# Performance work log

Hardware: AMD Instinct MI355X
Metric: run time of the kernel (lower is better)

Reference implementation:

```python
import jax, jax.numpy as jnp
import numpy as np


def _min_gru_layer(h_in, Wz, bz, Wh, bh):
    # h_in: [B, T, D_in]; gates/candidate via two GEMMs
    z = jax.nn.sigmoid(jnp.einsum('btd,dh->bth', h_in, Wz) + bz)  # [B,T,H]
    h_tilde = jnp.einsum('btd,dh->bth', h_in, Wh) + bh            # [B,T,H]
    # Recurrence h_t = a_t * h_{t-1} + b_t with a_t = 1-z_t, b_t = z_t*h_tilde.
    # h_0 = 0 (frozen zeros param in the torch module), so the associative
    # scan over (a, b) directly yields h_t for t = 1..T.
    a = 1.0 - z
    b = z * h_tilde

    def combine(c1, c2):
        a1, b1 = c1
        a2, b2 = c2
        return a1 * a2, a2 * b1 + b2

    _, h = jax.lax.associative_scan(combine, (a, b), axis=1)
    return h


def setup_inputs() -> dict:
    key = jax.random.key(0)
    ks = jax.random.split(key, 8)
    B, T, Din, H, Dout = 8, 4096, 512, 1024, 512
    s_in = 1.0 / np.sqrt(Din)
    s_h = 1.0 / np.sqrt(H)
    return {
        'x':   jax.random.normal(ks[0], (B, T, Din), dtype=jnp.float32),
        'Wz0': jax.random.normal(ks[1], (Din, H), dtype=jnp.float32) * s_in,
        'bz0': jnp.zeros((H,), dtype=jnp.float32),
        'Wh0': jax.random.normal(ks[2], (Din, H), dtype=jnp.float32) * s_in,
        'bh0': jnp.zeros((H,), dtype=jnp.float32),
        'Wz1': jax.random.normal(ks[3], (H, H), dtype=jnp.float32) * s_h,
        'bz1': jnp.zeros((H,), dtype=jnp.float32),
        'Wh1': jax.random.normal(ks[4], (H, H), dtype=jnp.float32) * s_h,
        'bh1': jnp.zeros((H,), dtype=jnp.float32),
        'Wfc': jax.random.normal(ks[5], (H, Dout), dtype=jnp.float32) * s_h,
        'bfc': jnp.zeros((Dout,), dtype=jnp.float32),
    }


def reference(x, Wz0, bz0, Wh0, bh0, Wz1, bz1, Wh1, bh1, Wfc, bfc):
    h = _min_gru_layer(x, Wz0, bz0, Wh0, bh0)   # layer 0
    h = _min_gru_layer(h, Wz1, bz1, Wh1, bh1)   # layer 1
    return jnp.einsum('bth,ho->bto', h, Wfc) + bfc
```

## Files before the change

kernel.cpp:

```cpp
#include <hip/hip_runtime.h>

typedef __attribute__((ext_vector_type(4))) float fv4;
typedef __attribute__((ext_vector_type(8))) _Float16 hv8;
typedef __attribute__((ext_vector_type(4))) _Float16 hv4;
typedef __attribute__((ext_vector_type(2))) _Float16 hv2;

__device__ __forceinline__ void gload16(const void* g, void* l) {
  __builtin_amdgcn_global_load_lds(
      (const __attribute__((address_space(1))) unsigned int*)g,
      (__attribute__((address_space(3))) unsigned int*)l, 16, 0, 0);
}

struct GemmCore {
  const _Float16 *ap0, *bp0;
  size_t half;
  _Float16 *ldsA0, *ldsA1, *ldsB0, *ldsB1;
  const _Float16 *fa0, *fa1, *fb0, *fb1;
  int wave;

  __device__ __forceinline__ void init(const _Float16* A, const _Float16* Bt,
                                       _Float16* lds, int m0, int n0, int K,
                                       int tid) {
    wave = tid >> 6;
    const int lane = tid & 63;
    const int wm = (wave >> 1), wn = (wave & 1);
    const int quad = lane >> 4, r = lane & 15;
    ldsA0 = lds;         ldsA1 = lds + 4096;
    ldsB0 = lds + 8192;  ldsB1 = lds + 12288;
    const int cg = (tid & 3) ^ ((tid >> 3) & 3);
    ap0 = A  + (size_t)(m0 + (tid >> 2)) * K + cg * 8;
    bp0 = Bt + (size_t)(n0 + (tid >> 2)) * K + cg * 8;
    half = (size_t)64 * K;
    const int sq = quad ^ ((r >> 1) & 3);
    fa0 = ldsA0 + (wm * 64 + r) * 32 + sq * 8;
    fa1 = ldsA1 + (wm * 64 + r) * 32 + sq * 8;
    fb0 = ldsB0 + (wn * 64 + r) * 32 + sq * 8;
    fb1 = ldsB1 + (wn * 64 + r) * 32 + sq * 8;
  }

  __device__ __forceinline__ void run(fv4 acc[4][4], int K) {
    const int kiters = K >> 6;
    for (int kk = 0; kk < kiters; ++kk) {
      gload16(ap0,             ldsA0 + wave * 512);
      gload16(ap0 + half,      ldsA0 + wave * 512 + 2048);
      gload16(ap0 + 32,        ldsA1 + wave * 512);
      gload16(ap0 + half + 32, ldsA1 + wave * 512 + 2048);
      gload16(bp0,             ldsB0 + wave * 512);
      gload16(bp0 + half,      ldsB0 + wave * 512 + 2048);
      gload16(bp0 + 32,        ldsB1 + wave * 512);
      gload16(bp0 + half + 32, ldsB1 + wave * 512 + 2048);
      ap0 += 64; bp0 += 64;
      __syncthreads();

      hv8 av[4], bv[4];
#pragma unroll
      for (int t = 0; t < 4; ++t) {
        av[t] = *(const hv8*)(fa0 + t * 512);
        bv[t] = *(const hv8*)(fb0 + t * 512);
      }
#pragma unroll
      for (int tm = 0; tm < 4; ++tm)
#pragma unroll
        for (int tn = 0; tn < 4; ++tn)
          acc[tm][tn] = __builtin_amdgcn_mfma_f32_16x16x32_f16(av[tm], bv[tn],
                                                               acc[tm][tn], 0, 0, 0);
#pragma unroll
      for (int t = 0; t < 4; ++t) {
        av[t] = *(const hv8*)(fa1 + t * 512);
        bv[t] = *(const hv8*)(fb1 + t * 512);
      }
#pragma unroll
      for (int tm = 0; tm < 4; ++tm)
#pragma unroll
        for (int tn = 0; tn < 4; ++tn)
          acc[tm][tn] = __builtin_amdgcn_mfma_f32_16x16x32_f16(av[tm], bv[tn],
                                                               acc[tm][tn], 0, 0, 0);
      __syncthreads();
    }
  }
};

__device__ __forceinline__ void xcd_map(int bid, int ntl2, int mt_per_x,
                                        int& m0, int& n0) {
  const int xcd = bid & 7;
  const int k2  = bid >> 3;
  m0 = (xcd * mt_per_x + (k2 >> ntl2)) * 128;
  n0 = (k2 & ((1 << ntl2) - 1)) * 128;
}

__global__ __launch_bounds__(256)
void gemm_gate(const _Float16* __restrict__ A, const _Float16* __restrict__ Btf,
               _Float16* __restrict__ zh2,
               float* __restrict__ cA, float* __restrict__ cB,
               const float* __restrict__ bz, const float* __restrict__ bh,
               int K, int ntl2, int mt_per_x) {
  __shared__ _Float16 lds[4 * 128 * 32];
  const int tid  = threadIdx.x;
  const int lane = tid & 63;
  const int wave = tid >> 6;
  const int wm = wave >> 1, wn = wave & 1;
  const int quad = lane >> 4, r = lane & 15;
  int m0, n0;
  xcd_map(blockIdx.x, ntl2, mt_per_x, m0, n0);

  GemmCore core;
  core.init(A, Btf, lds, m0, n0, K, tid);
  fv4 acc[4][4] = {};
  core.run(acc, K);

  const int jb   = (n0 + wn * 64) >> 1;
  const int row0 = m0 + wm * 64 + quad * 4;
  const int cidx = (m0 >> 6) + wm;
#pragma unroll
  for (int tn = 0; tn < 2; ++tn) {
    const int j = jb + tn * 16 + r;
    const float bzv = bz[j];
    const float bhv = bh[j];
    float qA[4], qB[4];
#pragma unroll
    for (int tm = 0; tm < 4; ++tm) {
      float sA = 1.0f, sB = 0.0f;
#pragma unroll
      for (int r2 = 0; r2 < 4; ++r2) {
        const float zpre = acc[tm][tn][r2] + bzv;
        const float hpre = acc[tm][tn + 2][r2] + bhv;
        const float z = 1.0f / (1.0f + __expf(-zpre));
        const _Float16 a16 = (_Float16)(1.0f - z);
        const _Float16 b16 = (_Float16)(z * hpre);
        hv2 ab = {a16, b16};
        *(hv2*)(zh2 + ((size_t)(row0 + tm * 16 + r2) * 1024 + j) * 2) = ab;
        const float af = (float)a16, bf = (float)b16;
        sB = af * sB + bf;
        sA = sA * af;
      }
      qA[tm] = sA; qB[tm] = sB;
    }
#pragma unroll
    for (int tm = 0; tm < 4; ++tm) {
      float Av = qA[tm], Bv = qB[tm];
      float Ap = __shfl_up(Av, 16, 64);
      float Bp = __shfl_up(Bv, 16, 64);
      if (quad >= 1) { Bv = Av * Bp + Bv; Av = Ap * Av; }
      Ap = __shfl_up(Av, 32, 64);
      Bp = __shfl_up(Bv, 32, 64);
      if (quad >= 2) { Bv = Av * Bp + Bv; Av = Ap * Av; }
      qA[tm] = Av; qB[tm] = Bv;
    }
    if (quad == 3) {
      float CA = 1.0f, CB = 0.0f;
#pragma unroll
      for (int tm = 0; tm < 4; ++tm) { CB = qA[tm] * CB + qB[tm]; CA *= qA[tm]; }
      cA[(size_t)cidx * 1024 + j] = CA;
      cB[(size_t)cidx * 1024 + j] = CB;
    }
  }
}

__global__ __launch_bounds__(256)
void gemm_f16_bt(const _Float16* __restrict__ A, const _Float16* __restrict__ Bt,
                 float* __restrict__ C, const float* __restrict__ bias,
                 int N, int K, int ntl2, int mt_per_x) {
  __shared__ _Float16 lds[4 * 128 * 32];
  const int tid  = threadIdx.x;
  const int lane = tid & 63;
  const int wave = tid >> 6;
  const int wm = wave >> 1, wn = wave & 1;
  const int quad = lane >> 4, r = lane & 15;
  int m0, n0;
  xcd_map(blockIdx.x, ntl2, mt_per_x, m0, n0);

  GemmCore core;
  core.init(A, Bt, lds, m0, n0, K, tid);
  fv4 acc[4][4] = {};
  core.run(acc, K);

  const int col0 = n0 + wn * 64 + r;
  const int row0 = m0 + wm * 64 + quad * 4;
#pragma unroll
  for (int tn = 0; tn < 4; ++tn) {
    const int col = col0 + tn * 16;
    const float bs = bias[col];
#pragma unroll
    for (int tm = 0; tm < 4; ++tm) {
#pragma unroll
      for (int r2 = 0; r2 < 4; ++r2) {
        C[(size_t)(row0 + tm * 16 + r2) * N + col] = acc[tm][tn][r2] + bs;
      }
    }
  }
}

__global__ void cvt_f16(const float* __restrict__ x, _Float16* __restrict__ y) {
  size_t i = ((size_t)blockIdx.x * 256 + threadIdx.x) * 4;
  fv4 v = *(const fv4*)(x + i);
  *(hv4*)(y + i) = __builtin_convertvector(v, hv4);
}

__global__ void transpose_cvt(const float* __restrict__ W, _Float16* __restrict__ Wt,
                              int K, int N, int mult, int off) {
  __shared__ float tile[32][33];
  const int tx = threadIdx.x, ty = threadIdx.y;
  const int n  = blockIdx.x * 32 + tx;
  const int kb = blockIdx.y * 32;
  for (int i = ty; i < 32; i += 8)
    tile[i][tx] = W[(size_t)(kb + i) * N + n];
  __syncthreads();
  const int k = kb + tx;
  for (int i = ty; i < 32; i += 8)
    Wt[(size_t)(blockIdx.x * mult + off + i) * K + k] = (_Float16)tile[tx][i];
}

__global__ void scan_phaseB(const float* __restrict__ cA, const float* __restrict__ cB,
                            float* __restrict__ hcy) {
  const int gtid = blockIdx.x * 256 + threadIdx.x;
  const int lane = gtid & 63;
  const int wid  = gtid >> 6;
  const int h  = (wid & 255) * 4;
  const int bb = wid >> 8;
  const size_t o = (size_t)(bb * 64 + lane) * 1024 + h;
  fv4 Aa = *(const fv4*)(cA + o);
  fv4 Bv = *(const fv4*)(cB + o);
#pragma unroll
  for (int d = 1; d < 64; d <<= 1) {
    fv4 Ap, Bp;
#pragma unroll
    for (int k = 0; k < 4; ++k) {
      Ap[k] = __shfl_up(Aa[k], d, 64);
      Bp[k] = __shfl_up(Bv[k], d, 64);
    }
    if (lane >= d) {
      Bv = Aa * Bp + Bv;
      Aa = Ap * Aa;
    }
  }
  fv4 hc;
#pragma unroll
  for (int k = 0; k < 4; ++k) hc[k] = __shfl_up(Bv[k], 1, 64);
  if (lane == 0) { hc.x = 0.f; hc.y = 0.f; hc.z = 0.f; hc.w = 0.f; }
  *(fv4*)(hcy + o) = hc;
}

__global__ void scan_phaseC(const _Float16* __restrict__ zh2,
                            const float* __restrict__ hcy,
                            _Float16* __restrict__ hout) {
  const int idx = blockIdx.x * 256 + threadIdx.x;
  const int h  = (idx & 255) * 4;
  const int c  = (idx >> 8) & 63;
  const int bb = idx >> 14;
  const size_t base = ((size_t)(bb * 4096 + c * 64) * 1024 + h) * 2;
  const size_t ob   = (size_t)(bb * 4096 + c * 64) * 1024 + h;
  const size_t o    = (size_t)(bb * 64 + c) * 1024 + h;
  fv4 hc = *(const fv4*)(hcy + o);
#pragma unroll 4
  for (int t = 0; t < 64; ++t) {
    hv8 v = *(const hv8*)(zh2 + base + (size_t)t * 2048);
    fv4 av = __builtin_convertvector(__builtin_shufflevector(v, v, 0, 2, 4, 6), fv4);
    fv4 bv = __builtin_convertvector(__builtin_shufflevector(v, v, 1, 3, 5, 7), fv4);
    hc = av * hc + bv;
    *(hv4*)(hout + ob + (size_t)t * 1024) = __builtin_convertvector(hc, hv4);
  }
}

extern "C" void kernel_launch(void* const* d_in, const int* in_sizes, int n_in,
                              void* d_out, int out_size, void* d_ws, size_t ws_size,
                              hipStream_t stream) {
  const float* x   = (const float*)d_in[0];
  const float* Wz0 = (const float*)d_in[1];
  const float* bz0 = (const float*)d_in[2];
  const float* Wh0 = (const float*)d_in[3];
  const float* bh0 = (const float*)d_in[4];
  const float* Wz1 = (const float*)d_in[5];
  const float* bz1 = (const float*)d_in[6];
  const float* Wh1 = (const float*)d_in[7];
  const float* bh1 = (const float*)d_in[8];
  const float* Wfc = (const float*)d_in[9];
  const float* bfc = (const float*)d_in[10];

  const int Mrows = 32768;
  const int H = 1024, Din = 512, Dout = 512;

  char* w = (char*)d_ws;
  _Float16* zh2   = (_Float16*)w; w += (size_t)Mrows * 2 * H * 2;
  _Float16* hx    = (_Float16*)w; w += (size_t)Mrows * H * 2;
  _Float16* Wzh0t = (_Float16*)w; w += (size_t)2 * H * Din * 2;
  _Float16* Wzh1t = (_Float16*)w; w += (size_t)2 * H * H * 2;
  _Float16* Wft   = (_Float16*)w; w += (size_t)Dout * H * 2;
  float*    cA    = (float*)w;    w += (size_t)8 * 64 * H * 4;
  float*    cB    = (float*)w;    w += (size_t)8 * 64 * H * 4;
  float*    hcy   = (float*)w;    w += (size_t)8 * 64 * H * 4;
  _Float16* Xb    = hx;

  cvt_f16<<<Mrows * Din / 1024, 256, 0, stream>>>(x, Xb);
  transpose_cvt<<<dim3(H / 32, Din / 32), dim3(32, 8), 0, stream>>>(Wz0, Wzh0t, Din, H, 64, 0);
  transpose_cvt<<<dim3(H / 32, Din / 32), dim3(32, 8), 0, stream>>>(Wh0, Wzh0t, Din, H, 64, 32);
  transpose_cvt<<<dim3(H / 32, H / 32),   dim3(32, 8), 0, stream>>>(Wz1, Wzh1t, H, H, 64, 0);
  transpose_cvt<<<dim3(H / 32, H / 32),   dim3(32, 8), 0, stream>>>(Wh1, Wzh1t, H, H, 64, 32);
  transpose_cvt<<<dim3(Dout / 32, H / 32), dim3(32, 8), 0, stream>>>(Wfc, Wft, H, Dout, 32, 0);

  gemm_gate<<<4096, 256, 0, stream>>>(Xb, Wzh0t, zh2, cA, cB, bz0, bh0, Din, 4, 32);
  scan_phaseB<<<512, 256, 0, stream>>>(cA, cB, hcy);
  scan_phaseC<<<512, 256, 0, stream>>>(zh2, hcy, hx);

  gemm_gate<<<4096, 256, 0, stream>>>(hx, Wzh1t, zh2, cA, cB, bz1, bh1, H, 4, 32);
  scan_phaseB<<<512, 256, 0, stream>>>(cA, cB, hcy);
  scan_phaseC<<<512, 256, 0, stream>>>(zh2, hcy, hx);

  gemm_f16_bt<<<1024, 256, 0, stream>>>(hx, Wft, (float*)d_out, bfc, Dout, H, 2, 32);
}
```

Baseline: 551.3 us.

## Enlarge GEMM tiles to 256x256 with 8 waves and 4-stage LDS pipeline

Replaces the 128x128 tile GEMM core with a 256x256 tile run by 512 threads (8 waves, each computing 128x64). It adds a 4-deep ring of LDS stages with explicit vmcnt waits so global-to-LDS loads overlap MFMA work, and raises wave priority during the MFMA burst. The intent is more data reuse per byte loaded and better latency hiding. In exchange it uses 128KB of LDS and many more accumulator registers per block, which lowers occupancy. It also reduces the grid to 1024/256 blocks, which may leave tail imbalance across CUs.

```diff
diff --git a/kernel.cpp b/kernel.cpp
--- a/kernel.cpp
+++ b/kernel.cpp
@@ -11,72 +11,81 @@
       (__attribute__((address_space(3))) unsigned int*)l, 16, 0, 0);
 }
 
-struct GemmCore {
-  const _Float16 *ap0, *bp0;
-  size_t half;
-  _Float16 *ldsA0, *ldsA1, *ldsB0, *ldsB1;
-  const _Float16 *fa0, *fa1, *fb0, *fb1;
-  int wave;
+struct GemmCore256 {
+  const _Float16 *ap, *bp;
+  size_t rstep;
+  _Float16* ls;
+  const _Float16 *fa, *fb;
+  int wv;
 
   __device__ __forceinline__ void init(const _Float16* A, const _Float16* Bt,
                                        _Float16* lds, int m0, int n0, int K,
                                        int tid) {
-    wave = tid >> 6;
+    ls = lds;
+    wv = tid >> 6;
     const int lane = tid & 63;
-    const int wm = (wave >> 1), wn = (wave & 1);
+    const int wm = wv >> 2, wn = wv & 3;
     const int quad = lane >> 4, r = lane & 15;
-    ldsA0 = lds;         ldsA1 = lds + 4096;
-    ldsB0 = lds + 8192;  ldsB1 = lds + 12288;
     const int cg = (tid & 3) ^ ((tid >> 3) & 3);
-    ap0 = A  + (size_t)(m0 + (tid >> 2)) * K + cg * 8;
-    bp0 = Bt + (size_t)(n0 + (tid >> 2)) * K + cg * 8;
-    half = (size_t)64 * K;
+    ap = A  + (size_t)(m0 + (tid >> 2)) * K + cg * 8;
+    bp = Bt + (size_t)(n0 + (tid >> 2)) * K + cg * 8;
+    rstep = (size_t)128 * K;
     const int sq = quad ^ ((r >> 1) & 3);
-    fa0 = ldsA0 + (wm * 64 + r) * 32 + sq * 8;
-    fa1 = ldsA1 + (wm * 64 + r) * 32 + sq * 8;
-    fb0 = ldsB0 + (wn * 64 + r) * 32 + sq * 8;
-    fb1 = ldsB1 + (wn * 64 + r) * 32 + sq * 8;
-  }
-
-  __device__ __forceinline__ void run(fv4 acc[4][4], int K) {
-    const int kiters = K >> 6;
-    for (int kk = 0; kk < kiters; ++kk) {
-      gload16(ap0,             ldsA0 + wave * 512);
-      gload16(ap0 + half,      ldsA0 + wave * 512 + 2048);
-      gload16(ap0 + 32,        ldsA1 + wave * 512);
-      gload16(ap0 + half + 32, ldsA1 + wave * 512 + 2048);
-      gload16(bp0,             ldsB0 + wave * 512);
-      gload16(bp0 + half,      ldsB0 + wave * 512 + 2048);
-      gload16(bp0 + 32,        ldsB1 + wave * 512);
-      gload16(bp0 + half + 32, ldsB1 + wave * 512 + 2048);
-      ap0 += 64; bp0 += 64;
-      __syncthreads();
-
-      hv8 av[4], bv[4];
-#pragma unroll
-      for (int t = 0; t < 4; ++t) {
-        av[t] = *(const hv8*)(fa0 + t * 512);
-        bv[t] = *(const hv8*)(fb0 + t * 512);
-      }
-#pragma unroll
-      for (int tm = 0; tm < 4; ++tm)
-#pragma unroll
-        for (int tn = 0; tn < 4; ++tn)
-          acc[tm][tn] = __builtin_amdgcn_mfma_f32_16x16x32_f16(av[tm], bv[tn],
-                                                               acc[tm][tn], 0, 0, 0);
-#pragma unroll
-      for (int t = 0; t < 4; ++t) {
-        av[t] = *(const hv8*)(fa1 + t * 512);
-        bv[t] = *(const hv8*)(fb1 + t * 512);
-      }
-#pragma unroll
-      for (int tm = 0; tm < 4; ++tm)
-#pragma unroll
-        for (int tn = 0; tn < 4; ++tn)
-          acc[tm][tn] = __builtin_amdgcn_mfma_f32_16x16x32_f16(av[tm], bv[tn],
-                                                               acc[tm][tn], 0, 0, 0);
-      __syncthreads();
-    }
+    fa = ls + (wm * 128 + r) * 32 + sq * 8;
+    fb = ls + 8192 + (wn * 64 + r) * 32 + sq * 8;
+  }
+
+  __device__ __forceinline__ void stage(int s) {
+    _Float16* d = ls + (s & 3) * 16384 + wv * 512;
+    const _Float16* a = ap + (size_t)s * 32;
+    const _Float16* b = bp + (size_t)s * 32;
+    gload16(a,         d);
+    gload16(a + rstep, d + 4096);
+    gload16(b,         d + 8192);
+    gload16(b + rstep, d + 12288);
+  }
+
+  template <int VM>
+  __device__ __forceinline__ void body(fv4 acc[8][4], int s) {
+    asm volatile("s_waitcnt vmcnt(%0)" :: "n"(VM) : "memory");
+    __builtin_amdgcn_s_barrier();
+    __builtin_amdgcn_sched_barrier(0);
+    const _Float16* fA = fa + (s & 3) * 16384;
+    const _Float16* fB = fb + (s & 3) * 16384;
+    hv8 a0[4], b0[4], a1[4];
+#pragma unroll
+    for (int t = 0; t < 4; ++t) a0[t] = *(const hv8*)(fA + t * 512);
+#pragma unroll
+    for (int t = 0; t < 4; ++t) b0[t] = *(const hv8*)(fB + t * 512);
+#pragma unroll
+    for (int t = 0; t < 4; ++t) a1[t] = *(const hv8*)(fA + (t + 4) * 512);
+    __builtin_amdgcn_s_setprio(1);
+#pragma unroll
+    for (int tm = 0; tm < 4; ++tm)
+#pragma unroll
+      for (int tn = 0; tn < 4; ++tn)
+        acc[tm][tn] = __builtin_amdgcn_mfma_f32_16x16x32_f16(a0[tm], b0[tn],
+                                                             acc[tm][tn], 0, 0, 0);
+#pragma unroll
+    for (int tm = 0; tm < 4; ++tm)
+#pragma unroll
+      for (int tn = 0; tn < 4; ++tn)
+        acc[tm + 4][tn] = __builtin_amdgcn_mfma_f32_16x16x32_f16(a1[tm], b0[tn],
+                                                                 acc[tm + 4][tn], 0, 0, 0);
+    __builtin_amdgcn_s_setprio(0);
+    asm volatile("s_waitcnt lgkmcnt(0)" ::: "memory");
+    __builtin_amdgcn_sched_barrier(0);
+    __builtin_amdgcn_s_barrier();
+  }
+
+  __device__ __forceinline__ void run(fv4 acc[8][4], int K) {
+    const int ns = K >> 5;
+    stage(0); stage(1); stage(2);
+    int s = 0;
+    for (; s < ns - 3; ++s) { stage(s + 3); body<12>(acc, s); }
+    body<8>(acc, s); ++s;
+    body<4>(acc, s); ++s;
+    body<0>(acc, s);
   }
 };
 
@@ -84,104 +93,108 @@
                                         int& m0, int& n0) {
   const int xcd = bid & 7;
   const int k2  = bid >> 3;
-  m0 = (xcd * mt_per_x + (k2 >> ntl2)) * 128;
-  n0 = (k2 & ((1 << ntl2) - 1)) * 128;
-}
-
-__global__ __launch_bounds__(256)
+  m0 = (xcd * mt_per_x + (k2 >> ntl2)) * 256;
+  n0 = (k2 & ((1 << ntl2) - 1)) * 256;
+}
+
+__global__ __launch_bounds__(512)
 void gemm_gate(const _Float16* __restrict__ A, const _Float16* __restrict__ Btf,
                _Float16* __restrict__ zh2,
                float* __restrict__ cA, float* __restrict__ cB,
                const float* __restrict__ bz, const float* __restrict__ bh,
                int K, int ntl2, int mt_per_x) {
-  __shared__ _Float16 lds[4 * 128 * 32];
+  __shared__ _Float16 lds[4 * 16384];
   const int tid  = threadIdx.x;
   const int lane = tid & 63;
   const int wave = tid >> 6;
-  const int wm = wave >> 1, wn = wave & 1;
+  const int wm = wave >> 2, wn = wave & 3;
   const int quad = lane >> 4, r = lane & 15;
   int m0, n0;
   xcd_map(blockIdx.x, ntl2, mt_per_x, m0, n0);
 
-  GemmCore core;
+  GemmCore256 core;
   core.init(A, Btf, lds, m0, n0, K, tid);
-  fv4 acc[4][4] = {};
+  fv4 acc[8][4] = {};
   core.run(acc, K);
 
   const int jb   = (n0 + wn * 64) >> 1;
-  const int row0 = m0 + wm * 64 + quad * 4;
-  const int cidx = (m0 >> 6) + wm;
+  const int row0 = m0 + wm * 128 + quad * 4;
+  const int cb   = (m0 >> 6) + wm * 2;
 #pragma unroll
   for (int tn = 0; tn < 2; ++tn) {
     const int j = jb + tn * 16 + r;
     const float bzv = bz[j];
     const float bhv = bh[j];
-    float qA[4], qB[4];
-#pragma unroll
-    for (int tm = 0; tm < 4; ++tm) {
-      float sA = 1.0f, sB = 0.0f;
-#pragma unroll
-      for (int r2 = 0; r2 < 4; ++r2) {
-        const float zpre = acc[tm][tn][r2] + bzv;
-        const float hpre = acc[tm][tn + 2][r2] + bhv;
-        const float z = 1.0f / (1.0f + __expf(-zpre));
-        const _Float16 a16 = (_Float16)(1.0f - z);
-        const _Float16 b16 = (_Float16)(z * hpre);
-        hv2 ab = {a16, b16};
-        *(hv2*)(zh2 + ((size_t)(row0 + tm * 16 + r2) * 1024 + j) * 2) = ab;
-        const float af = (float)a16, bf = (float)b16;
-        sB = af * sB + bf;
-        sA = sA * af;
+#pragma unroll
+    for (int tg = 0; tg < 2; ++tg) {
+      float qA[4], qB[4];
+#pragma unroll
+      for (int tq = 0; tq < 4; ++tq) {
+        const int tm = tg * 4 + tq;
+        float sA = 1.0f, sB = 0.0f;
+#pragma unroll
+        for (int r2 = 0; r2 < 4; ++r2) {
+          const float zpre = acc[tm][tn][r2] + bzv;
+          const float hpre = acc[tm][tn + 2][r2] + bhv;
+          const float z = 1.0f / (1.0f + __expf(-zpre));
+          const _Float16 a16 = (_Float16)(1.0f - z);
+          const _Float16 b16 = (_Float16)(z * hpre);
+          hv2 ab = {a16, b16};
+          *(hv2*)(zh2 + ((size_t)(row0 + tm * 16 + r2) * 1024 + j) * 2) = ab;
+          const float af = (float)a16, bf = (float)b16;
+          sB = af * sB + bf;
+          sA = sA * af;
+        }
+        qA[tq] = sA; qB[tq] = sB;
       }
-      qA[tm] = sA; qB[tm] = sB;
+#pragma unroll
+      for (int tq = 0; tq < 4; ++tq) {
+        float Av = qA[tq], Bv = qB[tq];
+        float Ap = __shfl_up(Av, 16, 64);
+        float Bp = __shfl_up(Bv, 16, 64);
+        if (quad >= 1) { Bv = Av * Bp + Bv; Av = Ap * Av; }
+        Ap = __shfl_up(Av, 32, 64);
+        Bp = __shfl_up(Bv, 32, 64);
+        if (quad >= 2) { Bv = Av * Bp + Bv; Av = Ap * Av; }
+        qA[tq] = Av; qB[tq] = Bv;
+      }
+      if (quad == 3) {
+        float CA = 1.0f, CB = 0.0f;
+#pragma unroll
+        for (int tq = 0; tq < 4; ++tq) { CB = qA[tq] * CB + qB[tq]; CA *= qA[tq]; }
+        cA[(size_t)(cb + tg) * 1024 + j] = CA;
+        cB[(size_t)(cb + tg) * 1024 + j] = CB;
+      }
     }
-#pragma unroll
-    for (int tm = 0; tm < 4; ++tm) {
-      float Av = qA[tm], Bv = qB[tm];
-      float Ap = __shfl_up(Av, 16, 64);
-      float Bp = __shfl_up(Bv, 16, 64);
-      if (quad >= 1) { Bv = Av * Bp + Bv; Av = Ap * Av; }
-      Ap = __shfl_up(Av, 32, 64);
-      Bp = __shfl_up(Bv, 32, 64);
-      if (quad >= 2) { Bv = Av * Bp + Bv; Av = Ap * Av; }
-      qA[tm] = Av; qB[tm] = Bv;
-    }
-    if (quad == 3) {
-      float CA = 1.0f, CB = 0.0f;
-#pragma unroll
-      for (int tm = 0; tm < 4; ++tm) { CB = qA[tm] * CB + qB[tm]; CA *= qA[tm]; }
-      cA[(size_t)cidx * 1024 + j] = CA;
-      cB[(size_t)cidx * 1024 + j] = CB;
-    }
-  }
-}
-
-__global__ __launch_bounds__(256)
+  }
+}
+
+__global__ __launch_bounds__(512)
 void gemm_f16_bt(const _Float16* __restrict__ A, const _Float16* __restrict__ Bt,
                  float* __restrict__ C, const float* __restrict__ bias,
                  int N, int K, int ntl2, int mt_per_x) {
-  __shared__ _Float16 lds[4 * 128 * 32];
+  __shared__ _Float16 lds[4 * 16384];
   const int tid  = threadIdx.x;
   const int lane = tid & 63;
   const int wave = tid >> 6;
-  const int wm = wave >> 1, wn = wave & 1;
+  const int wm = wave >> 2, wn = wave & 3;
   const int quad = lane >> 4, r = lane & 15;
   int m0, n0;
   xcd_map(blockIdx.x, ntl2, mt_per_x, m0, n0);
 
-  GemmCore core;
+  GemmCore256 core;
   core.init(A, Bt, lds, m0, n0, K, tid);
-  fv4 acc[4][4] = {};
+  fv4 acc[8][4] = {};
   core.run(acc, K);
 
   const int col0 = n0 + wn * 64 + r;
-  const int row0 = m0 + wm * 64 + quad * 4;
+  const int row0 = m0 + wm * 128 + quad * 4;
 #pragma unroll
   for (int tn = 0; tn < 4; ++tn) {
     const int col = col0 + tn * 16;
     const float bs = bias[col];
 #pragma unroll
-    for (int tm = 0; tm < 4; ++tm) {
+    for (int tm = 0; tm < 8; ++tm) {
 #pragma unroll
       for (int r2 = 0; r2 < 4; ++r2) {
         C[(size_t)(row0 + tm * 16 + r2) * N + col] = acc[tm][tn][r2] + bs;
@@ -297,13 +310,13 @@
   transpose_cvt<<<dim3(H / 32, H / 32),   dim3(32, 8), 0, stream>>>(Wh1, Wzh1t, H, H, 64, 32);
   transpose_cvt<<<dim3(Dout / 32, H / 32), dim3(32, 8), 0, stream>>>(Wfc, Wft, H, Dout, 32, 0);
 
-  gemm_gate<<<4096, 256, 0, stream>>>(Xb, Wzh0t, zh2, cA, cB, bz0, bh0, Din, 4, 32);
+  gemm_gate<<<1024, 512, 0, stream>>>(Xb, Wzh0t, zh2, cA, cB, bz0, bh0, Din, 3, 16);
   scan_phaseB<<<512, 256, 0, stream>>>(cA, cB, hcy);
   scan_phaseC<<<512, 256, 0, stream>>>(zh2, hcy, hx);
 
-  gemm_gate<<<4096, 256, 0, stream>>>(hx, Wzh1t, zh2, cA, cB, bz1, bh1, H, 4, 32);
+  gemm_gate<<<1024, 512, 0, stream>>>(hx, Wzh1t, zh2, cA, cB, bz1, bh1, H, 3, 16);
   scan_phaseB<<<512, 256, 0, stream>>>(cA, cB, hcy);
   scan_phaseC<<<512, 256, 0, stream>>>(zh2, hcy, hx);
 
-  gemm_f16_bt<<<1024, 256, 0, stream>>>(hx, Wft, (float*)d_out, bfc, Dout, H, 2, 32);
-}
+  gemm_f16_bt<<<256, 512, 0, stream>>>(hx, Wft, (float*)d_out, bfc, Dout, H, 1, 16);
+}
```

Result: faster. 506.6 us (-8.1%).
